# Kernel tuning notes

Hardware: AMD Instinct MI355X
Metric: run time of the kernel (lower is better)

The kernel has to match this reference:

```python
import jax, jax.numpy as jnp
import numpy as np

IMG = 512
C = 3
PS = 16
G = 32
B = 64
NH = IMG // PS
NW = IMG // PS
NP_ = NH * NW
P2 = PS * PS


def setup_inputs() -> dict:
    key = jax.random.key(0)
    k1, k2, k3, k4 = jax.random.split(key, 4)
    x = jax.random.normal(k1, (B, C, IMG, IMG), dtype=jnp.float32)
    # Conv2d(1, ps*ps, kernel=ps) default init ~ U(-1/ps, 1/ps); scale random normals similarly.
    obfuscation_weights = jax.random.normal(k2, (C, G, P2, P2), dtype=jnp.float32) / PS
    obfuscation_biases = jax.random.normal(k3, (C, G, P2), dtype=jnp.float32) / PS
    channel_permutation = jax.random.permutation(k4, jnp.arange(C, dtype=jnp.int32))
    return {
        "x": x,
        "obfuscation_weights": obfuscation_weights,
        "obfuscation_biases": obfuscation_biases,
        "channel_permutation": channel_permutation,
    }


def reference(x, obfuscation_weights, obfuscation_biases, channel_permutation):
    # x: (B, C, H, W) -> patches (B, C, N, ps*ps)
    x_patched = (
        x.reshape(B, C, NH, PS, NW, PS)
        .transpose(0, 1, 2, 4, 3, 5)
        .reshape(B, C, NP_, P2)
    )
    # group index per spatial patch: (row + col) % group_size
    ridx = jnp.arange(NH)[:, None]
    cidx = jnp.arange(NW)[None, :]
    group_map = ((ridx + cidx) % G).reshape(-1)  # (N,)
    sel_w = obfuscation_weights[:, group_map]  # (C, N, P2, P2)
    sel_b = obfuscation_biases[:, group_map]  # (C, N, P2)
    out = jnp.einsum("bcnp,cnpo->bcno", x_patched, sel_w) + sel_b
    # back to image layout
    out = (
        out.reshape(B, C, NH, NW, PS, PS)
        .transpose(0, 1, 2, 4, 3, 5)
        .reshape(B, C, IMG, IMG)
    )
    out = out[:, channel_permutation]
    return jnp.tanh(out)
```

## Files before the change

### kernel.cpp

```cpp
#include <hip/hip_runtime.h>

#define C_SZ   3
#define IMG_SZ 512
#define G_SZ   32
#define P2_SZ  256

typedef short  short8 __attribute__((ext_vector_type(8)));
typedef float  f32x4  __attribute__((ext_vector_type(4)));
typedef unsigned short u16;
typedef u16    u16x8  __attribute__((ext_vector_type(8)));

__device__ __forceinline__ u16 f2bf(float f) {
    unsigned u = __float_as_uint(f);
    u += 0x7FFFu + ((u >> 16) & 1u);
    return (u16)(u >> 16);
}

__device__ __forceinline__ float tanh_fast(float v) {
    float e = __expf(2.f * v);
    return 1.f - 2.f * __builtin_amdgcn_rcpf(e + 1.f);
}

__global__ __launch_bounds__(256)
void prep_wt(const float* __restrict__ w, u16* __restrict__ wt) {
    const int cg = blockIdx.x;
    const int pt = blockIdx.y;
    const int ot = blockIdx.z;
    __shared__ float T[64][68];
    const int tid = threadIdx.x;
    const float* wb = w + (size_t)cg * 65536 + (size_t)(pt * 64) * 256 + ot * 64;
    #pragma unroll
    for (int pass = 0; pass < 4; ++pass) {
        int q  = pass * 256 + tid;
        int pl = q >> 4, o4 = (q & 15) * 4;
        float4 v = *reinterpret_cast<const float4*>(wb + (size_t)pl * 256 + o4);
        T[pl][o4 + 0] = v.x; T[pl][o4 + 1] = v.y;
        T[pl][o4 + 2] = v.z; T[pl][o4 + 3] = v.w;
    }
    __syncthreads();
    const int pch = tid & 3, ol = tid >> 2;
    u16x8 v0, v1;
    #pragma unroll
    for (int j = 0; j < 8; ++j)  v0[j] = f2bf(T[pch * 16 + j][ol]);
    #pragma unroll
    for (int j = 0; j < 8; ++j)  v1[j] = f2bf(T[pch * 16 + 8 + j][ol]);
    u16* dst = wt + (size_t)cg * 65536 + (size_t)(ot * 64 + ol) * 256 + pt * 64 + pch * 16;
    *reinterpret_cast<u16x8*>(dst)     = v0;
    *reinterpret_cast<u16x8*>(dst + 8) = v1;
}

__global__ __launch_bounds__(256, 2)
void obf_mfma(const float* __restrict__ x,
              const u16*  __restrict__ wt,
              const float* __restrict__ bias,
              const int*  __restrict__ perm,
              float* __restrict__ out)
{
    const int mtile = blockIdx.x;
    const int cg    = blockIdx.z;
    const int c = cg >> 5, g = cg & 31;
    const int tid  = threadIdx.x;
    const int lane = tid & 63, wv = tid >> 6;

    __shared__ u16 As[64][40];
    __shared__ u16 Bs[256][40];

    f32x4 acc[4][4] = {};

    int cp = 0;
    #pragma unroll
    for (int i = 0; i < C_SZ; ++i) if (perm[i] == c) cp = i;

    const float* a_src[2];
    int a_ml[2], a_half[2], a_f4[2];
    #pragma unroll
    for (int pass = 0; pass < 2; ++pass) {
        int q    = pass * 256 + tid;
        int ml   = q >> 3, half = (q >> 2) & 1, f4 = q & 3;
        int mg   = mtile * 64 + ml;
        int b    = mg >> 5, nh = mg & 31, nw = (g - nh) & 31;
        a_src[pass] = x + (((size_t)(b * C_SZ + c) * IMG_SZ + nh * 16 + half) * IMG_SZ
                           + nw * 16 + f4 * 4);
        a_ml[pass] = ml; a_half[pass] = half; a_f4[pass] = f4;
    }
    const u16* b_src[4];
    int b_n[4], b_ch[4];
    const u16* wtb = wt + (size_t)cg * 65536;
    #pragma unroll
    for (int pass = 0; pass < 4; ++pass) {
        int q = pass * 256 + tid;
        b_n[pass] = q >> 2; b_ch[pass] = q & 3;
        b_src[pass] = wtb + (size_t)b_n[pass] * 256 + b_ch[pass] * 8;
    }

    for (int ks = 0; ks < 8; ++ks) {
        #pragma unroll
        for (int pass = 0; pass < 2; ++pass) {
            float4 v = *reinterpret_cast<const float4*>(a_src[pass] + (size_t)ks * 2 * IMG_SZ);
            u16* d = &As[a_ml[pass]][a_half[pass] * 16 + a_f4[pass] * 4];
            d[0] = f2bf(v.x); d[1] = f2bf(v.y); d[2] = f2bf(v.z); d[3] = f2bf(v.w);
        }
        #pragma unroll
        for (int pass = 0; pass < 4; ++pass) {
            uint4 v = *reinterpret_cast<const uint4*>(b_src[pass] + ks * 32);
            *reinterpret_cast<uint4*>(&Bs[b_n[pass]][b_ch[pass] * 8]) = v;
        }
        __syncthreads();

        short8 a[4], b[4];
        const int r = lane & 15, koff = (lane >> 4) * 8;
        #pragma unroll
        for (int mi = 0; mi < 4; ++mi)
            a[mi] = *reinterpret_cast<const short8*>(&As[mi * 16 + r][koff]);
        #pragma unroll
        for (int ni = 0; ni < 4; ++ni)
            b[ni] = *reinterpret_cast<const short8*>(&Bs[wv * 64 + ni * 16 + r][koff]);
        #pragma unroll
        for (int mi = 0; mi < 4; ++mi)
            #pragma unroll
            for (int ni = 0; ni < 4; ++ni)
                acc[mi][ni] = __builtin_amdgcn_mfma_f32_16x16x32_bf16(
                    a[mi], b[ni], acc[mi][ni], 0, 0, 0);
        __syncthreads();
    }

    const int cc = lane & 15;
    float bv[4];
    #pragma unroll
    for (int ni = 0; ni < 4; ++ni)
        bv[ni] = bias[(size_t)cg * 256 + wv * 64 + ni * 16 + cc];

    #pragma unroll
    for (int mi = 0; mi < 4; ++mi) {
        #pragma unroll
        for (int reg = 0; reg < 4; ++reg) {
            const int ml = mi * 16 + (lane >> 4) * 4 + reg;
            const int mg = mtile * 64 + ml;
            const int b  = mg >> 5, nh = mg & 31, nw = (g - nh) & 31;
            float* orow = out + ((size_t)(b * C_SZ + cp) * IMG_SZ + nh * 16) * IMG_SZ
                              + nw * 16 + cc;
            #pragma unroll
            for (int ni = 0; ni < 4; ++ni) {
                const int rp = wv * 4 + ni;
                orow[(size_t)rp * IMG_SZ] = tanh_fast(acc[mi][ni][reg] + bv[ni]);
            }
        }
    }
}

extern "C" void kernel_launch(void* const* d_in, const int* in_sizes, int n_in,
                              void* d_out, int out_size, void* d_ws, size_t ws_size,
                              hipStream_t stream) {
    const float* x    = (const float*)d_in[0];
    const float* w    = (const float*)d_in[1];
    const float* bias = (const float*)d_in[2];
    const int*   perm = (const int*)d_in[3];
    float* out = (float*)d_out;
    u16*   wt  = (u16*)d_ws;

    dim3 pgrid(C_SZ * G_SZ, 4, 4);
    prep_wt<<<pgrid, 256, 0, stream>>>(w, wt);

    dim3 grid(32, 1, C_SZ * G_SZ);
    obf_mfma<<<grid, 256, 0, stream>>>(x, wt, bias, perm, out);
}
```

Measured before the change: 150.3 us.

## Pre-swizzle weights into MFMA fragment layout and double-buffer A with register prefetch

The weight prep kernel now writes bf16 weights already in per-lane MFMA fragment order, so the main kernel loads B fragments straight from global memory into registers and drops the B shared-memory tile. The A tile is double-buffered in LDS, with the next k-step of x and weights prefetched into registers while the current MFMAs run. The grid is flattened and remapped so neighbouring blocks are spread across channel-groups, and occupancy is raised to three blocks per SM. Register pressure grows from the prefetch buffers, and direct global B loads depend on cache hits for weight reuse across blocks.

```diff
diff --git a/kernel.cpp b/kernel.cpp
--- a/kernel.cpp
+++ b/kernel.cpp
@@ -3,7 +3,6 @@
 #define C_SZ   3
 #define IMG_SZ 512
 #define G_SZ   32
-#define P2_SZ  256
 
 typedef short  short8 __attribute__((ext_vector_type(8)));
 typedef float  f32x4  __attribute__((ext_vector_type(4)));
@@ -24,46 +23,47 @@
 __global__ __launch_bounds__(256)
 void prep_wt(const float* __restrict__ w, u16* __restrict__ wt) {
     const int cg = blockIdx.x;
-    const int pt = blockIdx.y;
-    const int ot = blockIdx.z;
-    __shared__ float T[64][68];
+    const int kb = blockIdx.y;
+    __shared__ float T[32][260];
     const int tid = threadIdx.x;
-    const float* wb = w + (size_t)cg * 65536 + (size_t)(pt * 64) * 256 + ot * 64;
+    const float* wb = w + (size_t)cg * 65536 + (size_t)kb * 32 * 256;
     #pragma unroll
-    for (int pass = 0; pass < 4; ++pass) {
-        int q  = pass * 256 + tid;
-        int pl = q >> 4, o4 = (q & 15) * 4;
+    for (int pass = 0; pass < 8; ++pass) {
+        int q = pass * 256 + tid;
+        int pl = q >> 6, o4 = (q & 63) * 4;
         float4 v = *reinterpret_cast<const float4*>(wb + (size_t)pl * 256 + o4);
         T[pl][o4 + 0] = v.x; T[pl][o4 + 1] = v.y;
         T[pl][o4 + 2] = v.z; T[pl][o4 + 3] = v.w;
     }
     __syncthreads();
-    const int pch = tid & 3, ol = tid >> 2;
-    u16x8 v0, v1;
+    u16* dst = wt + ((size_t)cg * 8 + kb) * 8192;
     #pragma unroll
-    for (int j = 0; j < 8; ++j)  v0[j] = f2bf(T[pch * 16 + j][ol]);
-    #pragma unroll
-    for (int j = 0; j < 8; ++j)  v1[j] = f2bf(T[pch * 16 + 8 + j][ol]);
-    u16* dst = wt + (size_t)cg * 65536 + (size_t)(ot * 64 + ol) * 256 + pt * 64 + pch * 16;
-    *reinterpret_cast<u16x8*>(dst)     = v0;
-    *reinterpret_cast<u16x8*>(dst + 8) = v1;
+    for (int h0 = 0; h0 < 4; ++h0) {
+        int h = h0 * 256 + tid;
+        int kg = h >> 8, n = h & 255;
+        u16x8 v;
+        #pragma unroll
+        for (int e = 0; e < 8; ++e) v[e] = f2bf(T[kg * 8 + e][n]);
+        *reinterpret_cast<u16x8*>(dst + (size_t)kg * 2048 + n * 8) = v;
+    }
 }
 
-__global__ __launch_bounds__(256, 2)
+__global__ __launch_bounds__(256, 3)
 void obf_mfma(const float* __restrict__ x,
               const u16*  __restrict__ wt,
               const float* __restrict__ bias,
               const int*  __restrict__ perm,
               float* __restrict__ out)
 {
-    const int mtile = blockIdx.x;
-    const int cg    = blockIdx.z;
+    const int bid  = blockIdx.x;
+    const int sbid = (bid & 7) * 384 + (bid >> 3);
+    const int mtile = sbid & 31;
+    const int cg    = sbid >> 5;
     const int c = cg >> 5, g = cg & 31;
     const int tid  = threadIdx.x;
     const int lane = tid & 63, wv = tid >> 6;
 
-    __shared__ u16 As[64][40];
-    __shared__ u16 Bs[256][40];
+    __shared__ u16 As[2][64][40];
 
     f32x4 acc[4][4] = {};
 
@@ -72,7 +72,7 @@
     for (int i = 0; i < C_SZ; ++i) if (perm[i] == c) cp = i;
 
     const float* a_src[2];
-    int a_ml[2], a_half[2], a_f4[2];
+    int a_off[2];
     #pragma unroll
     for (int pass = 0; pass < 2; ++pass) {
         int q    = pass * 256 + tid;
@@ -81,54 +81,68 @@
         int b    = mg >> 5, nh = mg & 31, nw = (g - nh) & 31;
         a_src[pass] = x + (((size_t)(b * C_SZ + c) * IMG_SZ + nh * 16 + half) * IMG_SZ
                            + nw * 16 + f4 * 4);
-        a_ml[pass] = ml; a_half[pass] = half; a_f4[pass] = f4;
+        a_off[pass] = ml * 40 + half * 16 + f4 * 4;
     }
-    const u16* b_src[4];
-    int b_n[4], b_ch[4];
-    const u16* wtb = wt + (size_t)cg * 65536;
+    const int r = lane & 15, kg = lane >> 4;
+    const u16* bsrc = wt + (size_t)cg * 65536 + kg * 2048 + ((size_t)(wv * 64 + r)) * 8;
+
+    f32x4 av[2];
+    av[0] = *reinterpret_cast<const f32x4*>(a_src[0]);
+    av[1] = *reinterpret_cast<const f32x4*>(a_src[1]);
+    short8 bfrag[4];
     #pragma unroll
-    for (int pass = 0; pass < 4; ++pass) {
-        int q = pass * 256 + tid;
-        b_n[pass] = q >> 2; b_ch[pass] = q & 3;
-        b_src[pass] = wtb + (size_t)b_n[pass] * 256 + b_ch[pass] * 8;
+    for (int ni = 0; ni < 4; ++ni)
+        bfrag[ni] = *reinterpret_cast<const short8*>(bsrc + ni * 128);
+    #pragma unroll
+    for (int pass = 0; pass < 2; ++pass) {
+        u16* d = &As[0][0][0] + a_off[pass];
+        d[0] = f2bf(av[pass][0]); d[1] = f2bf(av[pass][1]);
+        d[2] = f2bf(av[pass][2]); d[3] = f2bf(av[pass][3]);
     }
+    __syncthreads();
 
+    const int koff = kg * 8;
+    #pragma unroll
     for (int ks = 0; ks < 8; ++ks) {
-        #pragma unroll
-        for (int pass = 0; pass < 2; ++pass) {
-            float4 v = *reinterpret_cast<const float4*>(a_src[pass] + (size_t)ks * 2 * IMG_SZ);
-            u16* d = &As[a_ml[pass]][a_half[pass] * 16 + a_f4[pass] * 4];
-            d[0] = f2bf(v.x); d[1] = f2bf(v.y); d[2] = f2bf(v.z); d[3] = f2bf(v.w);
+        f32x4 an[2];
+        short8 bn[4];
+        if (ks < 7) {
+            an[0] = *reinterpret_cast<const f32x4*>(a_src[0] + (size_t)(ks + 1) * 2 * IMG_SZ);
+            an[1] = *reinterpret_cast<const f32x4*>(a_src[1] + (size_t)(ks + 1) * 2 * IMG_SZ);
+            #pragma unroll
+            for (int ni = 0; ni < 4; ++ni)
+                bn[ni] = *reinterpret_cast<const short8*>(bsrc + (ks + 1) * 8192 + ni * 128);
         }
-        #pragma unroll
-        for (int pass = 0; pass < 4; ++pass) {
-            uint4 v = *reinterpret_cast<const uint4*>(b_src[pass] + ks * 32);
-            *reinterpret_cast<uint4*>(&Bs[b_n[pass]][b_ch[pass] * 8]) = v;
-        }
-        __syncthreads();
-
-        short8 a[4], b[4];
-        const int r = lane & 15, koff = (lane >> 4) * 8;
+        const u16* abase = &As[ks & 1][0][0];
+        short8 a[4];
         #pragma unroll
         for (int mi = 0; mi < 4; ++mi)
-            a[mi] = *reinterpret_cast<const short8*>(&As[mi * 16 + r][koff]);
-        #pragma unroll
-        for (int ni = 0; ni < 4; ++ni)
-            b[ni] = *reinterpret_cast<const short8*>(&Bs[wv * 64 + ni * 16 + r][koff]);
+            a[mi] = *reinterpret_cast<const short8*>(abase + (mi * 16 + r) * 40 + koff);
         #pragma unroll
         for (int mi = 0; mi < 4; ++mi)
             #pragma unroll
             for (int ni = 0; ni < 4; ++ni)
                 acc[mi][ni] = __builtin_amdgcn_mfma_f32_16x16x32_bf16(
-                    a[mi], b[ni], acc[mi][ni], 0, 0, 0);
+                    a[mi], bfrag[ni], acc[mi][ni], 0, 0, 0);
+        if (ks < 7) {
+            u16* d0 = &As[(ks & 1) ^ 1][0][0];
+            #pragma unroll
+            for (int pass = 0; pass < 2; ++pass) {
+                u16* d = d0 + a_off[pass];
+                d[0] = f2bf(an[pass][0]); d[1] = f2bf(an[pass][1]);
+                d[2] = f2bf(an[pass][2]); d[3] = f2bf(an[pass][3]);
+            }
+            #pragma unroll
+            for (int ni = 0; ni < 4; ++ni) bfrag[ni] = bn[ni];
+        }
         __syncthreads();
     }
 
     const int cc = lane & 15;
-    float bv[4];
+    float bs[4];
     #pragma unroll
     for (int ni = 0; ni < 4; ++ni)
-        bv[ni] = bias[(size_t)cg * 256 + wv * 64 + ni * 16 + cc];
+        bs[ni] = bias[(size_t)cg * 256 + wv * 64 + ni * 16 + cc];
 
     #pragma unroll
     for (int mi = 0; mi < 4; ++mi) {
@@ -142,7 +156,7 @@
             #pragma unroll
             for (int ni = 0; ni < 4; ++ni) {
                 const int rp = wv * 4 + ni;
-                orow[(size_t)rp * IMG_SZ] = tanh_fast(acc[mi][ni][reg] + bv[ni]);
+                orow[(size_t)rp * IMG_SZ] = tanh_fast(acc[mi][ni][reg] + bs[ni]);
             }
         }
     }
@@ -158,9 +172,8 @@
     float* out = (float*)d_out;
     u16*   wt  = (u16*)d_ws;
 
-    dim3 pgrid(C_SZ * G_SZ, 4, 4);
+    dim3 pgrid(C_SZ * G_SZ, 8, 1);
     prep_wt<<<pgrid, 256, 0, stream>>>(w, wt);
 
-    dim3 grid(32, 1, C_SZ * G_SZ);
-    obf_mfma<<<grid, 256, 0, stream>>>(x, wt, bias, perm, out);
+    obf_mfma<<<3072, 256, 0, stream>>>(x, wt, bias, perm, out);
 }
```

New measurement: 149.8 us. No clear change (-0.3%).
